# Kernel tuning notes

Hardware: AMD Instinct MI355X
Metric: run time of the kernel (lower is better)

The kernel has to match this reference:

```python
import jax, jax.numpy as jnp
import numpy as np

N, E = 100000, 1600000          # nodes, edges
DIN, DH, DOUT = 128, 128, 64    # input_dim, hidden_dim, output_dim


def setup_inputs() -> dict:
    key = jax.random.key(0)
    k0, k1, k2, k3 = jax.random.split(key, 4)
    x = jax.random.normal(k0, (N, DIN), dtype=jnp.float32)
    edge_index = jax.random.randint(k1, (2, E), 0, N)
    # GCNConv params (glorot-ish weights, zero bias)
    W1 = jax.random.normal(k2, (DIN, DH), dtype=jnp.float32) / np.sqrt(DIN).astype(np.float32)
    b1 = jnp.zeros((DH,), jnp.float32)
    W2 = jax.random.normal(k3, (DH, DOUT), dtype=jnp.float32) / np.sqrt(DH).astype(np.float32)
    b2 = jnp.zeros((DOUT,), jnp.float32)
    return {"x": x, "edge_index": edge_index, "W1": W1, "b1": b1, "W2": W2, "b2": b2}


def _gcn_conv(h_in, W, b, src, dst, norm_e, self_norm, n):
    # PyG GCNConv: transform, then normalized sum-aggregation with self-loops.
    h = h_in @ W                                   # [N, dout]
    msg = h[src] * norm_e[:, None]                 # [E, dout] gather + edge scale
    agg = jax.ops.segment_sum(msg, dst, num_segments=n)
    agg = agg + h * self_norm[:, None]             # self-loop contribution (norm = 1/deg)
    return agg + b


def reference(x, edge_index, W1, b1, W2, b2):
    src, dst = edge_index[0], edge_index[1]
    n = x.shape[0]
    # degree including self-loop, computed on dst (PyG convention)
    deg = jax.ops.segment_sum(jnp.ones((src.shape[0],), x.dtype), dst, num_segments=n) + 1.0
    dinv = jax.lax.rsqrt(deg)
    norm_e = dinv[src] * dinv[dst]                 # per-edge D^-1/2 A D^-1/2
    self_norm = dinv * dinv
    h = _gcn_conv(x, W1, b1, src, dst, norm_e, self_norm, n)
    h = jax.nn.relu(h)                             # dropout is identity in eval mode
    out = _gcn_conv(h, W2, b2, src, dst, norm_e, self_norm, n)
    return out
```

## Files before the change

### kernel.cpp

```cpp
#include <hip/hip_runtime.h>

#define NN 100000
#define NE 1600000
#define NBUCK 1563
#define NBH 256
#define CHUNK 6250
#define NBXB 12500
#define NBG 1563


typedef short bf16x8 __attribute__((ext_vector_type(8)));
typedef float f32x4  __attribute__((ext_vector_type(4)));
typedef float f32x2  __attribute__((ext_vector_type(2)));

__device__ __forceinline__ float b2f(unsigned short u) {
    return __uint_as_float(((unsigned int)u) << 16);
}
__device__ __forceinline__ unsigned short f2b(float f) {
    unsigned int x = __float_as_uint(f);
    x += 0x7FFFu + ((x >> 16) & 1u);
    return (unsigned short)(x >> 16);
}

__global__ __launch_bounds__(256) void k_pre(const float* __restrict__ x,
                                             unsigned short* __restrict__ xb,
                                             const int* __restrict__ dst,
                                             int* __restrict__ ghist) {
    int b = blockIdx.x;
    if (b < NBXB) {
        int id = b * 256 + threadIdx.x;
        float4 v = ((const float4*)x)[id];
        ushort4 o;
        o.x = f2b(v.x); o.y = f2b(v.y); o.z = f2b(v.z); o.w = f2b(v.w);
        ((ushort4*)xb)[id] = o;
        return;
    }
    __shared__ int h[NBUCK];
    int tid = threadIdx.x;
    int i = b - NBXB;
    for (int k = tid; k < NBUCK; k += 256) h[k] = 0;
    __syncthreads();
    int e0 = i * CHUNK;
    for (int e = e0 + tid; e < e0 + CHUNK; e += 256) {
        unsigned d = (unsigned)dst[e];
        if (d < NN) atomicAdd(&h[d >> 6], 1);
    }
    __syncthreads();
    for (int k = tid; k < NBUCK; k += 256) ghist[i * NBUCK + k] = h[k];
}

__global__ __launch_bounds__(256) void k_scanB(const int* __restrict__ ghist,
                                               int* __restrict__ boffT,
                                               int* __restrict__ tot) {
    int k = blockIdx.x * 256 + threadIdx.x;
    if (k >= NBUCK) return;
    int sum = 0;
#pragma unroll 8
    for (int i = 0; i < NBH; ++i) {
        int c = ghist[i * NBUCK + k];
        boffT[i * NBUCK + k] = sum;
        sum += c;
    }
    tot[k] = sum;
}

__global__ __launch_bounds__(256) void k_scanT(const int* __restrict__ tot,
                                               int* __restrict__ bbase) {
    __shared__ int s[256];
    int tid = threadIdx.x;
    int k0 = tid * 7;
    int v[7]; int S = 0;
#pragma unroll
    for (int q = 0; q < 7; ++q) {
        int k = k0 + q;
        v[q] = (k < NBUCK) ? tot[k] : 0;
        S += v[q];
    }
    s[tid] = S;
    __syncthreads();
    for (int off = 1; off < 256; off <<= 1) {
        int t = (tid >= off) ? s[tid - off] : 0;
        __syncthreads();
        s[tid] += t;
        __syncthreads();
    }
    int run = s[tid] - S;
#pragma unroll
    for (int q = 0; q < 7; ++q) {
        int k = k0 + q;
        if (k < NBUCK) { bbase[k] = run; run += v[q]; }
    }
}

__global__ __launch_bounds__(256) void k_place(const int* __restrict__ src,
                                               const int* __restrict__ dst,
                                               const int* __restrict__ bbase,
                                               const int* __restrict__ boffT,
                                               int* __restrict__ ebuf) {
    __shared__ int cur[NBUCK];
    int tid = threadIdx.x, i = blockIdx.x;
    for (int k = tid; k < NBUCK; k += 256)
        cur[k] = bbase[k] + boffT[i * NBUCK + k];
    __syncthreads();
    int e0 = i * CHUNK;
    for (int e = e0 + tid; e < e0 + CHUNK; e += 256) {
        unsigned d = (unsigned)dst[e];
        if (d >= NN) continue;
        unsigned s = (unsigned)src[e];
        if (s >= NN) s = 0;
        int pos = atomicAdd(&cur[d >> 6], 1);
        ebuf[pos] = (int)(s | ((d & 63u) << 17));
    }
}

__global__ __launch_bounds__(256) void k_binC(const int* __restrict__ bbase,
                                              const int* __restrict__ tot,
                                              const int* __restrict__ ebuf,
                                              int* __restrict__ row_start,
                                              float* __restrict__ dinv,
                                              int* __restrict__ csr) {
    __shared__ int cnt[64], excl[64], cur[64];
    int b = blockIdx.x, tid = threadIdx.x;
    int n0 = b * 64;
    int base = bbase[b], end = base + tot[b];
    if (tid < 64) cnt[tid] = 0;
    __syncthreads();
    for (int i = base + tid; i < end; i += 256)
        atomicAdd(&cnt[((unsigned)ebuf[i]) >> 17], 1);
    __syncthreads();
    if (tid == 0) {
        int run = 0;
        for (int t = 0; t < 64; ++t) { excl[t] = run; run += cnt[t]; }
    }
    __syncthreads();
    if (tid < 64) {
        int node = n0 + tid;
        if (node < NN) {
            row_start[node] = base + excl[tid];
            dinv[node] = rsqrtf((float)cnt[tid] + 1.0f);
        }
        cur[tid] = base + excl[tid];
    }
    if (b == NBUCK - 1 && tid == 0) row_start[NN] = end;
    __syncthreads();
    for (int i = base + tid; i < end; i += 256) {
        unsigned rec = (unsigned)ebuf[i];
        int pos = atomicAdd(&cur[rec >> 17], 1);
        csr[pos] = (int)(rec & 0x1FFFFu);
    }
}

__global__ __launch_bounds__(256) void k_agg1(const unsigned short* __restrict__ xb,
                                              const float* __restrict__ dinv,
                                              const int* __restrict__ row_start,
                                              const int* __restrict__ csr,
                                              char* __restrict__ P) {
    int node = blockIdx.x * 4 + (threadIdx.x >> 6);
    int lane = threadIdx.x & 63;
    int sub  = lane >> 4;
    int dimb = lane & 15;
    const uint4* X4 = (const uint4*)xb;
    float dv = dinv[node];
    float sn4 = dv * dv * 0.25f;
    uint4 sv = X4[(size_t)node * 16 + dimb];
    f32x2 a0, a1, a2, a3;
    a0.x = __uint_as_float(sv.x << 16) * sn4;  a0.y = __uint_as_float(sv.x & 0xFFFF0000u) * sn4;
    a1.x = __uint_as_float(sv.y << 16) * sn4;  a1.y = __uint_as_float(sv.y & 0xFFFF0000u) * sn4;
    a2.x = __uint_as_float(sv.z << 16) * sn4;  a2.y = __uint_as_float(sv.z & 0xFFFF0000u) * sn4;
    a3.x = __uint_as_float(sv.w << 16) * sn4;  a3.y = __uint_as_float(sv.w & 0xFFFF0000u) * sn4;
    int base = row_start[node], end = row_start[node + 1];
    for (int c0 = base; c0 < end; c0 += 64) {
        int idx = c0 + lane;
        int cl = min(idx, end - 1);
        int s = csr[cl];
        float wv = (idx < end) ? dinv[s] * dv : 0.f;
        int ng = min(64, end - c0);
        for (int g = 0; g * 4 < ng; ++g) {
            int   sq = __shfl(s,  g * 4 + sub);
            float wq = __shfl(wv, g * 4 + sub);
            uint4 v = X4[(size_t)sq * 16 + dimb];
            f32x2 wv2; wv2.x = wq; wv2.y = wq;
            f32x2 xv;
            xv.x = __uint_as_float(v.x << 16); xv.y = __uint_as_float(v.x & 0xFFFF0000u);
            a0 = __builtin_elementwise_fma(xv, wv2, a0);
            xv.x = __uint_as_float(v.y << 16); xv.y = __uint_as_float(v.y & 0xFFFF0000u);
            a1 = __builtin_elementwise_fma(xv, wv2, a1);
            xv.x = __uint_as_float(v.z << 16); xv.y = __uint_as_float(v.z & 0xFFFF0000u);
            a2 = __builtin_elementwise_fma(xv, wv2, a2);
            xv.x = __uint_as_float(v.w << 16); xv.y = __uint_as_float(v.w & 0xFFFF0000u);
            a3 = __builtin_elementwise_fma(xv, wv2, a3);
        }
    }
#pragma unroll
    for (int mgap = 16; mgap < 64; mgap <<= 1) {
        a0.x += __shfl_xor(a0.x, mgap); a0.y += __shfl_xor(a0.y, mgap);
        a1.x += __shfl_xor(a1.x, mgap); a1.y += __shfl_xor(a1.y, mgap);
        a2.x += __shfl_xor(a2.x, mgap); a2.y += __shfl_xor(a2.y, mgap);
        a3.x += __shfl_xor(a3.x, mgap); a3.y += __shfl_xor(a3.y, mgap);
    }
    if (lane < 16) {
        uint4 o;
        o.x = (unsigned)f2b(a0.x) | ((unsigned)f2b(a0.y) << 16);
        o.y = (unsigned)f2b(a1.x) | ((unsigned)f2b(a1.y) << 16);
        o.z = (unsigned)f2b(a2.x) | ((unsigned)f2b(a2.y) << 16);
        o.w = (unsigned)f2b(a3.x) | ((unsigned)f2b(a3.y) << 16);
        ((uint4*)(P + (size_t)node * 256))[lane] = o;
    }
}

__global__ __launch_bounds__(256) void k_gemm12(const float* __restrict__ W1,
                                                const float* __restrict__ b1,
                                                const float* __restrict__ W2,
                                                char* __restrict__ P) {
    __shared__ short Wl1[16384];
    __shared__ short Wl2[8192];
    __shared__ __align__(16) short Cl[4][16][128];
    const int tid = threadIdx.x;
    const int w = tid >> 6, lane = tid & 63;
    const int r0 = blockIdx.x * 64;

    for (int i = tid; i < 16384; i += 256) {
        int j = i & 7, l = (i >> 3) & 63, ks = (i >> 9) & 3, ct = i >> 11;
        int k = ks * 32 + ((l >> 4) << 3) + j;
        int c = ct * 16 + (l & 15);
        Wl1[i] = (short)f2b(W1[k * 128 + c]);
    }
    for (int i = tid; i < 8192; i += 256) {
        int j = i & 7, l = (i >> 3) & 63, ks = (i >> 9) & 3, ct = i >> 11;
        int k = ks * 32 + ((l >> 4) << 3) + j;
        int c = ct * 16 + (l & 15);
        Wl2[i] = (short)f2b(W2[k * 64 + c]);
    }
    __syncthreads();

    const int m = r0 + w * 16 + (lane & 15);
    const int quad = lane >> 4;
    const bool mok = (m < NN);
    bf16x8 a[4];
#pragma unroll
    for (int ks = 0; ks < 4; ++ks) {
        if (mok) a[ks] = *(const bf16x8*)(P + (size_t)m * 256 + (ks * 32 + quad * 8) * 2);
        else     a[ks] = bf16x8{0,0,0,0,0,0,0,0};
    }
#pragma unroll
    for (int ct = 0; ct < 8; ++ct) {
        f32x4 c = {0.f, 0.f, 0.f, 0.f};
#pragma unroll
        for (int ks = 0; ks < 4; ++ks) {
            bf16x8 b = *(const bf16x8*)&Wl1[((ct * 4 + ks) * 64 + lane) * 8];
            c = __builtin_amdgcn_mfma_f32_16x16x32_bf16(a[ks], b, c, 0, 0, 0);
        }
        int col = ct * 16 + (lane & 15);
        float bias = b1[col];
#pragma unroll
        for (int r = 0; r < 4; ++r)
            Cl[w][quad * 4 + r][col] = (short)f2b(fmaxf(c[r] + bias, 0.f));
    }
    __syncthreads();
    bf16x8 a2[4];
#pragma unroll
    for (int ks = 0; ks < 4; ++ks)
        a2[ks] = *(const bf16x8*)&Cl[w][lane & 15][ks * 32 + quad * 8];
    __syncthreads();
    short* Ct = &Cl[0][0][0];
#pragma unroll
    for (int ct = 0; ct < 4; ++ct) {
        f32x4 c = {0.f, 0.f, 0.f, 0.f};
#pragma unroll
        for (int ks = 0; ks < 4; ++ks) {
            bf16x8 b = *(const bf16x8*)&Wl2[((ct * 4 + ks) * 64 + lane) * 8];
            c = __builtin_amdgcn_mfma_f32_16x16x32_bf16(a2[ks], b, c, 0, 0, 0);
        }
        int col = ct * 16 + (lane & 15);
#pragma unroll
        for (int r = 0; r < 4; ++r)
            Ct[(w * 16 + quad * 4 + r) * 64 + col] = (short)f2b(c[r]);
    }
    __syncthreads();
    for (int it = 0; it < 8; ++it) {
        int row = it * 2 + (lane >> 5), u = lane & 31;
        int node = r0 + w * 16 + row;
        if (node < NN)
            *(unsigned int*)(P + (size_t)node * 256 + u * 4) =
                ((const unsigned int*)&Ct[(w * 16 + row) * 64])[u];
    }
}

__global__ __launch_bounds__(256) void k_agg2(const float* __restrict__ dinv,
                                              const int* __restrict__ row_start,
                                              const int* __restrict__ csr,
                                              const char* __restrict__ P,
                                              const float* __restrict__ b2,
                                              float* __restrict__ outp) {
    int node = blockIdx.x * 4 + (threadIdx.x >> 6);
    int lane = threadIdx.x & 63;
    int sub  = lane >> 3;
    int dimb = lane & 7;
    const uint4* P4 = (const uint4*)P;
    float dv = dinv[node];
    float sn8 = dv * dv * 0.125f;
    uint4 sv = P4[(size_t)node * 16 + dimb];
    f32x2 a0, a1, a2, a3;
    a0.x = __uint_as_float(sv.x << 16) * sn8;  a0.y = __uint_as_float(sv.x & 0xFFFF0000u) * sn8;
    a1.x = __uint_as_float(sv.y << 16) * sn8;  a1.y = __uint_as_float(sv.y & 0xFFFF0000u) * sn8;
    a2.x = __uint_as_float(sv.z << 16) * sn8;  a2.y = __uint_as_float(sv.z & 0xFFFF0000u) * sn8;
    a3.x = __uint_as_float(sv.w << 16) * sn8;  a3.y = __uint_as_float(sv.w & 0xFFFF0000u) * sn8;
    int base = row_start[node], end = row_start[node + 1];
    if (end > base) {
        for (int c0 = base; c0 < end; c0 += 64) {
            int idx = c0 + lane;
            int cl = min(idx, end - 1);
            int s = csr[cl];
            float wv = (idx < end) ? dinv[s] * dv : 0.f;
            int ng = min(64, end - c0);
            for (int g = 0; g * 8 < ng; ++g) {
                int   sq = __shfl(s,  g * 8 + sub);
                float wq = __shfl(wv, g * 8 + sub);
                uint4 v = P4[(size_t)sq * 16 + dimb];
                f32x2 wv2; wv2.x = wq; wv2.y = wq;
                f32x2 xv;
                xv.x = __uint_as_float(v.x << 16); xv.y = __uint_as_float(v.x & 0xFFFF0000u);
                a0 = __builtin_elementwise_fma(xv, wv2, a0);
                xv.x = __uint_as_float(v.y << 16); xv.y = __uint_as_float(v.y & 0xFFFF0000u);
                a1 = __builtin_elementwise_fma(xv, wv2, a1);
                xv.x = __uint_as_float(v.z << 16); xv.y = __uint_as_float(v.z & 0xFFFF0000u);
                a2 = __builtin_elementwise_fma(xv, wv2, a2);
                xv.x = __uint_as_float(v.w << 16); xv.y = __uint_as_float(v.w & 0xFFFF0000u);
                a3 = __builtin_elementwise_fma(xv, wv2, a3);
            }
        }
    }
#pragma unroll
    for (int mgap = 8; mgap < 64; mgap <<= 1) {
        a0.x += __shfl_xor(a0.x, mgap); a0.y += __shfl_xor(a0.y, mgap);
        a1.x += __shfl_xor(a1.x, mgap); a1.y += __shfl_xor(a1.y, mgap);
        a2.x += __shfl_xor(a2.x, mgap); a2.y += __shfl_xor(a2.y, mgap);
        a3.x += __shfl_xor(a3.x, mgap); a3.y += __shfl_xor(a3.y, mgap);
    }
    if (lane < 8) {
        float4 ba = ((const float4*)b2)[lane * 2];
        float4 bb = ((const float4*)b2)[lane * 2 + 1];
        float4 o0, o1;
        o0.x = a0.x + ba.x; o0.y = a0.y + ba.y; o0.z = a1.x + ba.z; o0.w = a1.y + ba.w;
        o1.x = a2.x + bb.x; o1.y = a2.y + bb.y; o1.z = a3.x + bb.z; o1.w = a3.y + bb.w;
        ((float4*)outp)[(size_t)node * 16 + lane * 2]     = o0;
        ((float4*)outp)[(size_t)node * 16 + lane * 2 + 1] = o1;
    }
}

extern "C" void kernel_launch(void* const* d_in, const int* in_sizes, int n_in,
                              void* d_out, int out_size, void* d_ws, size_t ws_size,
                              hipStream_t stream) {
    const float* x  = (const float*)d_in[0];
    const int*   ei = (const int*)d_in[1];
    const float* W1 = (const float*)d_in[2];
    const float* b1 = (const float*)d_in[3];
    const float* W2 = (const float*)d_in[4];
    const float* b2 = (const float*)d_in[5];
    float* out = (float*)d_out;
    const int* src = ei;
    const int* dst = ei + NE;

    char* ws = (char*)d_ws;
    unsigned short* xb        = (unsigned short*)(ws + 0);
    char*           P         = ws + 25600000;
    int*            ghist     = (int*)(ws + 25600000);
    int*            boffT     = (int*)(ws + 27200512);
    int*            tot       = (int*)(ws + 28801024);
    int*            bbase     = (int*)(ws + 28807276);
    int*            row_start = (int*)(ws + 51200000);
    float*          dinv      = (float*)(ws + 51600004);
    int*            csr       = (int*)(ws + 52000004);
    int*            ebuf      = (int*)(ws + 58400004);

    k_pre  <<<NBXB + NBH, 256, 0, stream>>>(x, xb, dst, ghist);
    k_scanB<<<(NBUCK + 255) / 256, 256, 0, stream>>>(ghist, boffT, tot);
    k_scanT<<<1, 256, 0, stream>>>(tot, bbase);
    k_place<<<NBH, 256, 0, stream>>>(src, dst, bbase, boffT, ebuf);
    k_binC <<<NBUCK, 256, 0, stream>>>(bbase, tot, ebuf, row_start, dinv, csr);

    k_agg1  <<<NN / 4, 256, 0, stream>>>(xb, dinv, row_start, csr, P);
    k_gemm12<<<NBG, 256, 0, stream>>>(W1, b1, W2, P);
    k_agg2  <<<NN / 4, 256, 0, stream>>>(dinv, row_start, csr, P, b2, out);
}
```

Measured before the change: 349.4 us.

## Fuse CSR build stages into one persistent kernel with grid barriers

The scan, bucket-offset, placement and per-bucket CSR kernels are merged into a single 512-block persistent kernel that uses atomic-counter grid barriers between phases. The histogram chunking also doubles to 512 blocks with half-size chunks, so the placement phase has more parallelism. The aim is to cut kernel launch gaps and tail effects in graph preprocessing. In exchange, the column scan over chunks doubles in length, ghist and boffT grow, and correctness relies on all 512 blocks being co-resident, since spin barriers can deadlock otherwise.

```diff
diff --git a/kernel.cpp b/kernel.cpp
--- a/kernel.cpp
+++ b/kernel.cpp
@@ -3,10 +3,11 @@
 #define NN 100000
 #define NE 1600000
 #define NBUCK 1563
-#define NBH 256
-#define CHUNK 6250
+#define NBH 512
+#define CHUNK 3125
 #define NBXB 12500
 #define NBG 1563
+#define NBB 512
 
 
 typedef short bf16x8 __attribute__((ext_vector_type(8)));
@@ -22,10 +23,22 @@
     return (unsigned short)(x >> 16);
 }
 
+__device__ __forceinline__ void gbar(int* bar, int idx, int n) {
+    __syncthreads();
+    if (threadIdx.x == 0) {
+        __threadfence();
+        atomicAdd(&bar[idx], 1);
+        while (atomicAdd(&bar[idx], 0) < n) __builtin_amdgcn_s_sleep(8);
+        __threadfence();
+    }
+    __syncthreads();
+}
+
 __global__ __launch_bounds__(256) void k_pre(const float* __restrict__ x,
                                              unsigned short* __restrict__ xb,
                                              const int* __restrict__ dst,
-                                             int* __restrict__ ghist) {
+                                             int* __restrict__ ghist,
+                                             int* __restrict__ bar) {
     int b = blockIdx.x;
     if (b < NBXB) {
         int id = b * 256 + threadIdx.x;
@@ -38,6 +51,7 @@
     __shared__ int h[NBUCK];
     int tid = threadIdx.x;
     int i = b - NBXB;
+    if (i == 0 && tid < 8) bar[tid] = 0;
     for (int k = tid; k < NBUCK; k += 256) h[k] = 0;
     __syncthreads();
     int e0 = i * CHUNK;
@@ -49,104 +63,109 @@
     for (int k = tid; k < NBUCK; k += 256) ghist[i * NBUCK + k] = h[k];
 }
 
-__global__ __launch_bounds__(256) void k_scanB(const int* __restrict__ ghist,
+__global__ __launch_bounds__(256) void k_build(const int* __restrict__ src,
+                                               const int* __restrict__ dst,
+                                               const int* __restrict__ ghist,
                                                int* __restrict__ boffT,
-                                               int* __restrict__ tot) {
-    int k = blockIdx.x * 256 + threadIdx.x;
-    if (k >= NBUCK) return;
-    int sum = 0;
+                                               int* __restrict__ tot,
+                                               int* __restrict__ bbase,
+                                               int* __restrict__ ebuf,
+                                               int* __restrict__ row_start,
+                                               float* __restrict__ dinv,
+                                               int* __restrict__ csr,
+                                               int* __restrict__ bar) {
+    __shared__ int cur[NBUCK];
+    __shared__ int s[256];
+    __shared__ int cnt[64], excl[64], cur4[64];
+    const int tid = threadIdx.x;
+
+    {
+        int k = blockIdx.x * 256 + tid;
+        if (k < NBUCK) {
+            int sum = 0;
 #pragma unroll 8
-    for (int i = 0; i < NBH; ++i) {
-        int c = ghist[i * NBUCK + k];
-        boffT[i * NBUCK + k] = sum;
-        sum += c;
-    }
-    tot[k] = sum;
-}
-
-__global__ __launch_bounds__(256) void k_scanT(const int* __restrict__ tot,
-                                               int* __restrict__ bbase) {
-    __shared__ int s[256];
-    int tid = threadIdx.x;
-    int k0 = tid * 7;
-    int v[7]; int S = 0;
-#pragma unroll
-    for (int q = 0; q < 7; ++q) {
-        int k = k0 + q;
-        v[q] = (k < NBUCK) ? tot[k] : 0;
-        S += v[q];
-    }
-    s[tid] = S;
-    __syncthreads();
-    for (int off = 1; off < 256; off <<= 1) {
-        int t = (tid >= off) ? s[tid - off] : 0;
-        __syncthreads();
-        s[tid] += t;
-        __syncthreads();
-    }
-    int run = s[tid] - S;
-#pragma unroll
-    for (int q = 0; q < 7; ++q) {
-        int k = k0 + q;
-        if (k < NBUCK) { bbase[k] = run; run += v[q]; }
-    }
-}
-
-__global__ __launch_bounds__(256) void k_place(const int* __restrict__ src,
-                                               const int* __restrict__ dst,
-                                               const int* __restrict__ bbase,
-                                               const int* __restrict__ boffT,
-                                               int* __restrict__ ebuf) {
-    __shared__ int cur[NBUCK];
-    int tid = threadIdx.x, i = blockIdx.x;
-    for (int k = tid; k < NBUCK; k += 256)
-        cur[k] = bbase[k] + boffT[i * NBUCK + k];
-    __syncthreads();
-    int e0 = i * CHUNK;
-    for (int e = e0 + tid; e < e0 + CHUNK; e += 256) {
-        unsigned d = (unsigned)dst[e];
-        if (d >= NN) continue;
-        unsigned s = (unsigned)src[e];
-        if (s >= NN) s = 0;
-        int pos = atomicAdd(&cur[d >> 6], 1);
-        ebuf[pos] = (int)(s | ((d & 63u) << 17));
-    }
-}
-
-__global__ __launch_bounds__(256) void k_binC(const int* __restrict__ bbase,
-                                              const int* __restrict__ tot,
-                                              const int* __restrict__ ebuf,
-                                              int* __restrict__ row_start,
-                                              float* __restrict__ dinv,
-                                              int* __restrict__ csr) {
-    __shared__ int cnt[64], excl[64], cur[64];
-    int b = blockIdx.x, tid = threadIdx.x;
-    int n0 = b * 64;
-    int base = bbase[b], end = base + tot[b];
-    if (tid < 64) cnt[tid] = 0;
-    __syncthreads();
-    for (int i = base + tid; i < end; i += 256)
-        atomicAdd(&cnt[((unsigned)ebuf[i]) >> 17], 1);
-    __syncthreads();
-    if (tid == 0) {
-        int run = 0;
-        for (int t = 0; t < 64; ++t) { excl[t] = run; run += cnt[t]; }
-    }
-    __syncthreads();
-    if (tid < 64) {
-        int node = n0 + tid;
-        if (node < NN) {
-            row_start[node] = base + excl[tid];
-            dinv[node] = rsqrtf((float)cnt[tid] + 1.0f);
-        }
-        cur[tid] = base + excl[tid];
-    }
-    if (b == NBUCK - 1 && tid == 0) row_start[NN] = end;
-    __syncthreads();
-    for (int i = base + tid; i < end; i += 256) {
-        unsigned rec = (unsigned)ebuf[i];
-        int pos = atomicAdd(&cur[rec >> 17], 1);
-        csr[pos] = (int)(rec & 0x1FFFFu);
+            for (int i = 0; i < NBH; ++i) {
+                int c = ghist[i * NBUCK + k];
+                boffT[i * NBUCK + k] = sum;
+                sum += c;
+            }
+            tot[k] = sum;
+        }
+    }
+    gbar(bar, 0, NBB);
+
+    if (blockIdx.x == 0) {
+        int k0 = tid * 7;
+        int v[7]; int S = 0;
+#pragma unroll
+        for (int q = 0; q < 7; ++q) {
+            int k = k0 + q;
+            v[q] = (k < NBUCK) ? tot[k] : 0;
+            S += v[q];
+        }
+        s[tid] = S;
+        __syncthreads();
+        for (int off = 1; off < 256; off <<= 1) {
+            int t = (tid >= off) ? s[tid - off] : 0;
+            __syncthreads();
+            s[tid] += t;
+            __syncthreads();
+        }
+        int run = s[tid] - S;
+#pragma unroll
+        for (int q = 0; q < 7; ++q) {
+            int k = k0 + q;
+            if (k < NBUCK) { bbase[k] = run; run += v[q]; }
+        }
+    }
+    gbar(bar, 1, NBB);
+
+    {
+        int i = blockIdx.x;
+        for (int k = tid; k < NBUCK; k += 256)
+            cur[k] = bbase[k] + boffT[i * NBUCK + k];
+        __syncthreads();
+        int e0 = i * CHUNK;
+        for (int e = e0 + tid; e < e0 + CHUNK; e += 256) {
+            unsigned d = (unsigned)dst[e];
+            if (d >= NN) continue;
+            unsigned sv = (unsigned)src[e];
+            if (sv >= NN) sv = 0;
+            int pos = atomicAdd(&cur[d >> 6], 1);
+            ebuf[pos] = (int)(sv | ((d & 63u) << 17));
+        }
+    }
+    gbar(bar, 2, NBB);
+
+    for (int b = blockIdx.x; b < NBUCK; b += NBB) {
+        int n0 = b * 64;
+        int base = bbase[b], end = base + tot[b];
+        if (tid < 64) cnt[tid] = 0;
+        __syncthreads();
+        for (int i = base + tid; i < end; i += 256)
+            atomicAdd(&cnt[((unsigned)ebuf[i]) >> 17], 1);
+        __syncthreads();
+        if (tid == 0) {
+            int run = 0;
+            for (int t = 0; t < 64; ++t) { excl[t] = run; run += cnt[t]; }
+        }
+        __syncthreads();
+        if (tid < 64) {
+            int node = n0 + tid;
+            if (node < NN) {
+                row_start[node] = base + excl[tid];
+                dinv[node] = rsqrtf((float)cnt[tid] + 1.0f);
+            }
+            cur4[tid] = base + excl[tid];
+        }
+        if (b == NBUCK - 1 && tid == 0) row_start[NN] = end;
+        __syncthreads();
+        for (int i = base + tid; i < end; i += 256) {
+            unsigned rec = (unsigned)ebuf[i];
+            int pos = atomicAdd(&cur4[rec >> 17], 1);
+            csr[pos] = (int)(rec & 0x1FFFFu);
+        }
+        __syncthreads();
     }
 }
 
@@ -365,19 +384,18 @@
     unsigned short* xb        = (unsigned short*)(ws + 0);
     char*           P         = ws + 25600000;
     int*            ghist     = (int*)(ws + 25600000);
-    int*            boffT     = (int*)(ws + 27200512);
-    int*            tot       = (int*)(ws + 28801024);
-    int*            bbase     = (int*)(ws + 28807276);
+    int*            boffT     = (int*)(ws + 28801024);
+    int*            tot       = (int*)(ws + 32002048);
+    int*            bbase     = (int*)(ws + 32008300);
     int*            row_start = (int*)(ws + 51200000);
     float*          dinv      = (float*)(ws + 51600004);
     int*            csr       = (int*)(ws + 52000004);
     int*            ebuf      = (int*)(ws + 58400004);
-
-    k_pre  <<<NBXB + NBH, 256, 0, stream>>>(x, xb, dst, ghist);
-    k_scanB<<<(NBUCK + 255) / 256, 256, 0, stream>>>(ghist, boffT, tot);
-    k_scanT<<<1, 256, 0, stream>>>(tot, bbase);
-    k_place<<<NBH, 256, 0, stream>>>(src, dst, bbase, boffT, ebuf);
-    k_binC <<<NBUCK, 256, 0, stream>>>(bbase, tot, ebuf, row_start, dinv, csr);
+    int*            bar       = (int*)(ws + 64800004);
+
+    k_pre  <<<NBXB + NBH, 256, 0, stream>>>(x, xb, dst, ghist, bar);
+    k_build<<<NBB, 256, 0, stream>>>(src, dst, ghist, boffT, tot, bbase,
+                                     ebuf, row_start, dinv, csr, bar);
 
     k_agg1  <<<NN / 4, 256, 0, stream>>>(xb, dinv, row_start, csr, P);
     k_gemm12<<<NBG, 256, 0, stream>>>(W1, b1, W2, P);
```

Measured after the change: 464.0 us. 32.8% more time.

## Parallelize bucket scan across segments and fold total scan into placement kernel

Applied to the files above, without the earlier changes.

The per-bucket column scan over 256 histogram rows is split into 8 segments handled by separate warps, with a shared-memory pass to combine segment prefixes. This raises the grid from 7 blocks to 49 and shortens each thread's serial chain. The single-block scan of bucket totals is removed as a separate launch; each placement block now recomputes that scan redundantly, and block 0 writes bbase for later kernels. Placement blocks are also remapped in an interleaved order. The cost is redundant scan work in every placement block and reading ghist twice in the column scan.

```diff
diff --git a/kernel.cpp b/kernel.cpp
--- a/kernel.cpp
+++ b/kernel.cpp
@@ -5,6 +5,8 @@
 #define NBUCK 1563
 #define NBH 256
 #define CHUNK 6250
+#define NSEG 8
+#define SEGC (NBH/NSEG)
 #define NBXB 12500
 #define NBG 1563
 
@@ -52,22 +54,43 @@
 __global__ __launch_bounds__(256) void k_scanB(const int* __restrict__ ghist,
                                                int* __restrict__ boffT,
                                                int* __restrict__ tot) {
-    int k = blockIdx.x * 256 + threadIdx.x;
-    if (k >= NBUCK) return;
-    int sum = 0;
+    __shared__ int part[NSEG][32];
+    int kk = threadIdx.x & 31, seg = threadIdx.x >> 5;
+    int k = blockIdx.x * 32 + kk;
+    bool ok = (k < NBUCK);
+    int i0 = seg * SEGC;
+    int S = 0;
+    if (ok) {
 #pragma unroll 8
-    for (int i = 0; i < NBH; ++i) {
-        int c = ghist[i * NBUCK + k];
-        boffT[i * NBUCK + k] = sum;
-        sum += c;
-    }
-    tot[k] = sum;
-}
-
-__global__ __launch_bounds__(256) void k_scanT(const int* __restrict__ tot,
-                                               int* __restrict__ bbase) {
+        for (int i = i0; i < i0 + SEGC; ++i) S += ghist[i * NBUCK + k];
+    }
+    part[seg][kk] = S;
+    __syncthreads();
+    int pre = 0;
+#pragma unroll
+    for (int s2 = 0; s2 < NSEG; ++s2) pre += (s2 < seg) ? part[s2][kk] : 0;
+    if (ok) {
+        int run = pre;
+#pragma unroll 8
+        for (int i = i0; i < i0 + SEGC; ++i) {
+            int c = ghist[i * NBUCK + k];
+            boffT[i * NBUCK + k] = run;
+            run += c;
+        }
+        if (seg == NSEG - 1) tot[k] = run;
+    }
+}
+
+__global__ __launch_bounds__(256) void k_place(const int* __restrict__ src,
+                                               const int* __restrict__ dst,
+                                               const int* __restrict__ tot,
+                                               const int* __restrict__ boffT,
+                                               int* __restrict__ ebuf,
+                                               int* __restrict__ bbase_out) {
+    __shared__ int cur[NBUCK];
     __shared__ int s[256];
-    int tid = threadIdx.x;
+    const int tid = threadIdx.x, bid = blockIdx.x;
+    const int i = ((bid & 7) * (NBH / 8)) + (bid >> 3);
     int k0 = tid * 7;
     int v[7]; int S = 0;
 #pragma unroll
@@ -88,28 +111,21 @@
 #pragma unroll
     for (int q = 0; q < 7; ++q) {
         int k = k0 + q;
-        if (k < NBUCK) { bbase[k] = run; run += v[q]; }
-    }
-}
-
-__global__ __launch_bounds__(256) void k_place(const int* __restrict__ src,
-                                               const int* __restrict__ dst,
-                                               const int* __restrict__ bbase,
-                                               const int* __restrict__ boffT,
-                                               int* __restrict__ ebuf) {
-    __shared__ int cur[NBUCK];
-    int tid = threadIdx.x, i = blockIdx.x;
-    for (int k = tid; k < NBUCK; k += 256)
-        cur[k] = bbase[k] + boffT[i * NBUCK + k];
+        if (k < NBUCK) {
+            cur[k] = run + boffT[i * NBUCK + k];
+            if (bid == 0) bbase_out[k] = run;
+            run += v[q];
+        }
+    }
     __syncthreads();
     int e0 = i * CHUNK;
     for (int e = e0 + tid; e < e0 + CHUNK; e += 256) {
         unsigned d = (unsigned)dst[e];
         if (d >= NN) continue;
-        unsigned s = (unsigned)src[e];
-        if (s >= NN) s = 0;
+        unsigned sv = (unsigned)src[e];
+        if (sv >= NN) sv = 0;
         int pos = atomicAdd(&cur[d >> 6], 1);
-        ebuf[pos] = (int)(s | ((d & 63u) << 17));
+        ebuf[pos] = (int)(sv | ((d & 63u) << 17));
     }
 }
 
@@ -374,9 +390,8 @@
     int*            ebuf      = (int*)(ws + 58400004);
 
     k_pre  <<<NBXB + NBH, 256, 0, stream>>>(x, xb, dst, ghist);
-    k_scanB<<<(NBUCK + 255) / 256, 256, 0, stream>>>(ghist, boffT, tot);
-    k_scanT<<<1, 256, 0, stream>>>(tot, bbase);
-    k_place<<<NBH, 256, 0, stream>>>(src, dst, bbase, boffT, ebuf);
+    k_scanB<<<(NBUCK + 31) / 32, 256, 0, stream>>>(ghist, boffT, tot);
+    k_place<<<NBH, 256, 0, stream>>>(src, dst, tot, boffT, ebuf, bbase);
     k_binC <<<NBUCK, 256, 0, stream>>>(bbase, tot, ebuf, row_start, dinv, csr);
 
     k_agg1  <<<NN / 4, 256, 0, stream>>>(xb, dinv, row_start, csr, P);
```

New measurement: 311.9 us. 10.8% less time.
